# Performance work log

Hardware: AMD Instinct MI355X
Metric: run time of the kernel (lower is better)

Reference implementation:

```python
import jax, jax.numpy as jnp
import numpy as np

B, C, H, W = 4, 256, 64, 64


def setup_inputs() -> dict:
    key = jax.random.key(0)
    ks = jax.random.split(key, 7)
    s = 1.0 / np.sqrt(C)
    return {
        "x": jax.random.normal(ks[0], (B, C, H, W), jnp.float32),
        "context": jax.random.normal(ks[1], (B, C, H, W), jnp.float32),
        "wq": jax.random.normal(ks[2], (C, C), jnp.float32) * s,
        "bq": jnp.zeros((C,), jnp.float32),
        "wk": jax.random.normal(ks[3], (C, C), jnp.float32) * s,
        "bk": jnp.zeros((C,), jnp.float32),
        "wv": jax.random.normal(ks[4], (C, C), jnp.float32) * s,
        "bv": jnp.zeros((C,), jnp.float32),
        "wo": jax.random.normal(ks[5], (C, C), jnp.float32) * s,
        "bo": jnp.zeros((C,), jnp.float32),
    }


def _proj(w, b, feats):
    # 1x1 conv == channel-mixing linear: feats [B,C,N] -> [B,C,N]
    return jnp.einsum("oc,bcn->bon", w, feats) + b[None, :, None]


def reference(x, context, wq, bq, wk, bk, wv, bv, wo, bo):
    b, c, h, w = x.shape
    xf = x.reshape(b, c, h * w)              # [B,C,Nq]
    cf = context.reshape(b, c, -1)           # [B,C,Nk]
    q = _proj(wq, bq, xf)                    # [B,C,Nq]
    k = _proj(wk, bk, cf)                    # [B,C,Nk]
    v = _proj(wv, bv, cf)                    # [B,C,Nk]
    attn = jnp.einsum("bci,bcj->bij", q, k)  # [B,Nq,Nk] = q^T k
    attn = jax.nn.softmax(attn, axis=-1)
    out = jnp.einsum("bcj,bij->bci", v, attn)  # v @ attn^T, [B,C,Nq]
    out = _proj(wo, bo, out).reshape(b, c, h, w)
    return out + x
```

## Files before the change

### kernel.cpp

```cpp
#include <hip/hip_runtime.h>

typedef _Float16 f16;
typedef _Float16 f16x8 __attribute__((ext_vector_type(8)));
typedef _Float16 f16x4 __attribute__((ext_vector_type(4)));
typedef float f32x4 __attribute__((ext_vector_type(4)));

#define DEVI __device__ __forceinline__

constexpr int B_ = 4, C_ = 256, N_ = 4096;

#define MFMAH(a, b, c) __builtin_amdgcn_mfma_f32_16x16x32_f16((a), (b), (c), 0, 0, 0)

DEVI void gload16(const void* g, void* l) {
  __builtin_amdgcn_global_load_lds((const __attribute__((address_space(1))) void*)g,
                                   (__attribute__((address_space(3))) void*)l, 16, 0, 0);
}

DEVI float bcast_row(float v0, float v1, float v2, float v3, int l15) {
  int src = (l15 >> 2) << 4;
  float a0 = __shfl(v0, src, 64);
  float a1 = __shfl(v1, src, 64);
  float a2 = __shfl(v2, src, 64);
  float a3 = __shfl(v3, src, 64);
  float x0 = (l15 & 1) ? a1 : a0;
  float x1 = (l15 & 1) ? a3 : a2;
  return (l15 & 2) ? x1 : x0;
}

__global__ __launch_bounds__(256, 1) void prep_weights(
    const float* __restrict__ wq, const float* __restrict__ wk,
    const float* __restrict__ wv, const float* __restrict__ wo,
    f16* __restrict__ wqh, f16* __restrict__ wkh,
    f16* __restrict__ wvh, f16* __restrict__ woh) {
  int idx = blockIdx.x * 256 + threadIdx.x;
  wqh[idx] = (f16)wq[idx];
  wkh[idx] = (f16)wk[idx];
  wvh[idx] = (f16)wv[idx];
  woh[idx] = (f16)wo[idx];
}

__global__ __launch_bounds__(256, 2) void proj_kv(
    const float* __restrict__ ctx, const float* __restrict__ bk, const float* __restrict__ bv,
    const f16* __restrict__ wkh, const f16* __restrict__ wvh,
    f16* __restrict__ KTh, f16* __restrict__ Vg) {
  const int blk = blockIdx.x;
  const int b = blk & 3;
  const int j0 = (blk >> 2) << 6;
  const int tid = threadIdx.x;
  const int lane = tid & 63;
  const int w = tid >> 6;
  const int l15 = lane & 15;
  const int g = lane >> 4;

  __shared__ alignas(16) f16 ldsC[64 * 256];

  {
    const float* cb = ctx + (size_t)b * C_ * N_ + j0;
    #pragma unroll
    for (int it = 0; it < 16; ++it) {
      int idx = it * 256 + tid;
      int c = idx >> 4;
      int j4 = (idx & 15) << 2;
      float4 f = *(const float4*)(cb + (size_t)c * N_ + j4);
      float vv[4] = {f.x, f.y, f.z, f.w};
      #pragma unroll
      for (int e = 0; e < 4; ++e) {
        int j = j4 + e;
        int uidx = j * 256 + ((((c >> 3) ^ (j & 7))) << 3) + (c & 7);
        ldsC[uidx] = (f16)vv[e];
      }
    }
  }
  __syncthreads();

  const int jloc = 16 * w + l15;
  f16x8 ch[8];
  #pragma unroll
  for (int ks = 0; ks < 8; ++ks)
    ch[ks] = *(const f16x8*)&ldsC[jloc * 256 + (((g + 4 * ks) ^ (jloc & 7)) << 3)];

  #pragma unroll 4
  for (int mt = 0; mt < 16; ++mt) {
    f32x4 ka = {0, 0, 0, 0}, va = {0, 0, 0, 0};
    #pragma unroll
    for (int ks = 0; ks < 8; ++ks) {
      int aoff = (16 * mt + l15) * 256 + 8 * g + 32 * ks;
      f16x8 ah = *(const f16x8*)(wkh + aoff);
      f16x8 av = *(const f16x8*)(wvh + aoff);
      ka = MFMAH(ah, ch[ks], ka);
      va = MFMAH(av, ch[ks], va);
    }
    int c0 = 16 * mt + 4 * g;
    float4 bk4 = *(const float4*)(bk + c0);
    float4 bv4 = *(const float4*)(bv + c0);
    f16x4 h4;
    #pragma unroll
    for (int r = 0; r < 4; ++r) h4[r] = (f16)(ka[r] + ((const float*)&bk4)[r]);
    *(f16x4*)(KTh + ((size_t)b * N_ + j0 + jloc) * C_ + c0) = h4;
    #pragma unroll
    for (int r = 0; r < 4; ++r) {
      float vv = va[r] + ((const float*)&bv4)[r];
      Vg[((size_t)b * C_ + c0 + r) * N_ + j0 + jloc] = (f16)vv;
    }
  }
}

DEVI void stageK(const f16* khg, int kv0, f16* ldsK, int w, int lane) {
  #pragma unroll
  for (int t = 0; t < 8; ++t) {
    int L = t * 256 + w * 64 + lane;
    int j = L >> 5, s = L & 31;
    const f16* src = khg + (size_t)(kv0 + j) * C_ + ((s ^ (j & 7)) << 3);
    gload16(src, ldsK + (size_t)(t * 256 + w * 64) * 8);
  }
}
DEVI void stageV(const f16* vg, int kv0, f16* ldsV, int w, int lane) {
  #pragma unroll
  for (int t = 0; t < 8; ++t) {
    int L = t * 256 + w * 64 + lane;
    int c = L >> 3, sl = L & 7;
    const f16* src = vg + (size_t)c * N_ + kv0 + ((sl ^ (c & 7)) << 3);
    gload16(src, ldsV + (size_t)(t * 256 + w * 64) * 8);
  }
}

__global__ __launch_bounds__(256, 1) void attn_fused(
    const float* __restrict__ x, const float* __restrict__ bq, const float* __restrict__ bo,
    const f16* __restrict__ wqh, const f16* __restrict__ woh,
    const f16* __restrict__ KTh, const f16* __restrict__ Vg,
    float* __restrict__ out) {
  const int blk = blockIdx.x;
  const int b = (blk & 7) >> 1;
  const int i0 = (((blk >> 3) << 1) | (blk & 1)) << 6;
  const int tid = threadIdx.x;
  const int lane = tid & 63;
  const int w = tid >> 6;
  const int l15 = lane & 15;
  const int g = lane >> 4;

  __shared__ alignas(16) char smem[140288];
  f16* ldsK0 = (f16*)smem;
  f16* ldsK1 = (f16*)(smem + 32768);
  f16* ldsV0 = (f16*)(smem + 65536);
  f16* ldsV1 = (f16*)(smem + 98304);
  f16* ldsPT = (f16*)(smem + 131072);

  {
    const float* xb = x + (size_t)b * C_ * N_ + i0;
    #pragma unroll
    for (int it = 0; it < 16; ++it) {
      int idx = it * 256 + tid;
      int c = idx >> 4;
      int i4 = (idx & 15) << 2;
      float4 f = *(const float4*)(xb + (size_t)c * N_ + i4);
      float vv[4] = {f.x, f.y, f.z, f.w};
      #pragma unroll
      for (int e = 0; e < 4; ++e) {
        int i = i4 + e;
        int uidx = i * 256 + ((((c >> 3) ^ (i & 7))) << 3) + (c & 7);
        ldsK0[uidx] = (f16)vv[e];
      }
    }
  }
  __syncthreads();

  const int iloc = 16 * w + l15;

  f16x8 xh[8];
  #pragma unroll
  for (int ks = 0; ks < 8; ++ks)
    xh[ks] = *(const f16x8*)&ldsK0[iloc * 256 + (((g + 4 * ks) ^ (iloc & 7)) << 3)];

  f32x4 qd[16];
  #pragma unroll
  for (int mt = 0; mt < 16; ++mt) {
    f32x4 a1 = {0, 0, 0, 0};
    #pragma unroll
    for (int ks = 0; ks < 8; ++ks) {
      f16x8 ah = *(const f16x8*)(wqh + (16 * mt + l15) * 256 + 8 * g + 32 * ks);
      a1 = MFMAH(ah, xh[ks], a1);
    }
    int c0 = 16 * mt + 4 * g;
    float4 bq4 = *(const float4*)(bq + c0);
    #pragma unroll
    for (int r = 0; r < 4; ++r) qd[mt][r] = a1[r] + ((const float*)&bq4)[r];
  }
  __syncthreads();

  #pragma unroll
  for (int mt = 0; mt < 16; ++mt) {
    int c0 = 16 * mt + 4 * g;
    f16x4 h4;
    #pragma unroll
    for (int r = 0; r < 4; ++r) h4[r] = (f16)qd[mt][r];
    *(f16x4*)&ldsK0[iloc * 256 + ((((c0 >> 3) ^ (iloc & 7))) << 3) + (c0 & 7)] = h4;
  }
  __syncthreads();

  f16x8 qh[8];
  #pragma unroll
  for (int ks = 0; ks < 8; ++ks)
    qh[ks] = *(const f16x8*)&ldsK0[iloc * 256 + (((g + 4 * ks) ^ (iloc & 7)) << 3)];
  __syncthreads();

  const f16* khg = KTh + (size_t)b * N_ * C_;
  const f16* vg = Vg + (size_t)b * C_ * N_;

  float mrun[4] = {-1e30f, -1e30f, -1e30f, -1e30f};
  float lrun[4] = {0, 0, 0, 0};
  f32x4 oacc[16];
  #pragma unroll
  for (int mt = 0; mt < 16; ++mt) oacc[mt] = (f32x4){0, 0, 0, 0};

  stageK(khg, 0, ldsK0, w, lane);
  stageV(vg, 0, ldsV0, w, lane);
  __syncthreads();

  for (int t = 0; t < 64; ++t) {
    const int kv0 = t << 6;
    f16* Kc = (t & 1) ? ldsK1 : ldsK0;
    f16* Vc = (t & 1) ? ldsV1 : ldsV0;
    f16* Kn = (t & 1) ? ldsK0 : ldsK1;
    f16* Vn = (t & 1) ? ldsV0 : ldsV1;

    if (t < 63) {
      stageK(khg, kv0 + 64, Kn, w, lane);
      stageV(vg, kv0 + 64, Vn, w, lane);
    }

    f32x4 s1[4];
    #pragma unroll
    for (int nt = 0; nt < 4; ++nt) s1[nt] = (f32x4){0, 0, 0, 0};
    #pragma unroll
    for (int ks = 0; ks < 8; ++ks) {
      f16x8 bh[4];
      #pragma unroll
      for (int nt = 0; nt < 4; ++nt) {
        int j = 16 * nt + l15;
        bh[nt] = *(const f16x8*)&Kc[j * 256 + (((g + 4 * ks) ^ (j & 7)) << 3)];
      }
      #pragma unroll
      for (int nt = 0; nt < 4; ++nt) s1[nt] = MFMAH(qh[ks], bh[nt], s1[nt]);
    }

    float tm[4];
    #pragma unroll
    for (int r = 0; r < 4; ++r) {
      tm[r] = fmaxf(fmaxf(s1[0][r], s1[1][r]), fmaxf(s1[2][r], s1[3][r]));
      #pragma unroll
      for (int msk = 1; msk < 16; msk <<= 1) tm[r] = fmaxf(tm[r], __shfl_xor(tm[r], msk));
    }
    bool grow = (tm[0] > mrun[0] + 6.f) | (tm[1] > mrun[1] + 6.f) |
                (tm[2] > mrun[2] + 6.f) | (tm[3] > mrun[3] + 6.f);
    float sc[4] = {1.f, 1.f, 1.f, 1.f};
    int need = __any((int)grow);
    if (need) {
      #pragma unroll
      for (int r = 0; r < 4; ++r) {
        float mn = fmaxf(mrun[r], tm[r]);
        sc[r] = __expf(mrun[r] - mn);
        mrun[r] = mn;
      }
      float fsc = bcast_row(sc[0], sc[1], sc[2], sc[3], l15);
      #pragma unroll
      for (int mt = 0; mt < 16; ++mt) oacc[mt] *= fsc;
    }
    float rs[4] = {0, 0, 0, 0};
    #pragma unroll
    for (int nt = 0; nt < 4; ++nt) {
      #pragma unroll
      for (int r = 0; r < 4; ++r) {
        float p = __expf(s1[nt][r] - mrun[r]);
        s1[nt][r] = p;
        rs[r] += p;
      }
    }
    #pragma unroll
    for (int r = 0; r < 4; ++r) {
      #pragma unroll
      for (int msk = 1; msk < 16; msk <<= 1) rs[r] += __shfl_xor(rs[r], msk);
      lrun[r] = need ? lrun[r] * sc[r] + rs[r] : lrun[r] + rs[r];
    }

    #pragma unroll
    for (int nt = 0; nt < 4; ++nt) {
      int jcol = 16 * nt + l15;
      #pragma unroll
      for (int r = 0; r < 4; ++r) ldsPT[w * 1152 + (4 * g + r) * 72 + jcol] = (f16)s1[nt][r];
    }
    f16x8 pb[2];
    #pragma unroll
    for (int ks2 = 0; ks2 < 2; ++ks2)
      pb[ks2] = *(const f16x8*)&ldsPT[w * 1152 + l15 * 72 + 8 * (g + 4 * ks2)];

    #pragma unroll
    for (int ks2 = 0; ks2 < 2; ++ks2) {
      #pragma unroll
      for (int mt = 0; mt < 16; ++mt) {
        int c = 16 * mt + l15;
        f16x8 va = *(const f16x8*)&Vc[c * 64 + (((g + 4 * ks2) ^ (c & 7)) << 3)];
        oacc[mt] = MFMAH(va, pb[ks2], oacc[mt]);
      }
    }

    __syncthreads();
  }

  {
    float inv[4];
    #pragma unroll
    for (int r = 0; r < 4; ++r) inv[r] = 1.0f / lrun[r];
    float fi = bcast_row(inv[0], inv[1], inv[2], inv[3], l15);
    #pragma unroll
    for (int mt = 0; mt < 16; ++mt) oacc[mt] *= fi;
  }
  #pragma unroll
  for (int mt = 0; mt < 16; ++mt) {
    int c0 = 16 * mt + 4 * g;
    f16x4 h4;
    #pragma unroll
    for (int r = 0; r < 4; ++r) h4[r] = (f16)oacc[mt][r];
    *(f16x4*)&ldsK0[iloc * 256 + ((((c0 >> 3) ^ (iloc & 7))) << 3) + (c0 & 7)] = h4;
  }
  __syncthreads();
  f32x4 facc[16];
  #pragma unroll
  for (int mt = 0; mt < 16; ++mt) facc[mt] = (f32x4){0, 0, 0, 0};
  #pragma unroll
  for (int ks = 0; ks < 8; ++ks) {
    f16x8 ob = *(const f16x8*)&ldsK0[iloc * 256 + (((g + 4 * ks) ^ (iloc & 7)) << 3)];
    #pragma unroll
    for (int mt = 0; mt < 16; ++mt) {
      f16x8 ah = *(const f16x8*)(woh + (16 * mt + l15) * 256 + 8 * g + 32 * ks);
      facc[mt] = MFMAH(ah, ob, facc[mt]);
    }
  }
  const int ig = i0 + iloc;
  #pragma unroll
  for (int mt = 0; mt < 16; ++mt) {
    int c0 = 16 * mt + 4 * g;
    float4 bo4 = *(const float4*)(bo + c0);
    #pragma unroll
    for (int r = 0; r < 4; ++r) {
      size_t off = ((size_t)b * C_ + c0 + r) * N_ + ig;
      out[off] = facc[mt][r] + ((const float*)&bo4)[r] + x[off];
    }
  }
}

extern "C" void kernel_launch(void* const* d_in, const int* in_sizes, int n_in,
                              void* d_out, int out_size, void* d_ws, size_t ws_size,
                              hipStream_t stream) {
  const float* x = (const float*)d_in[0];
  const float* ctx = (const float*)d_in[1];
  const float* wq = (const float*)d_in[2];
  const float* bq = (const float*)d_in[3];
  const float* wk = (const float*)d_in[4];
  const float* bk = (const float*)d_in[5];
  const float* wv = (const float*)d_in[6];
  const float* bv = (const float*)d_in[7];
  const float* wo = (const float*)d_in[8];
  const float* bo = (const float*)d_in[9];
  float* out = (float*)d_out;

  f16* ws = (f16*)d_ws;
  f16* wqh = ws;
  f16* wkh = wqh + 65536;
  f16* wvh = wkh + 65536;
  f16* woh = wvh + 65536;
  f16* KTh = woh + 65536;
  f16* Vg = KTh + (size_t)B_ * N_ * C_;

  prep_weights<<<256, 256, 0, stream>>>(wq, wk, wv, wo, wqh, wkh, wvh, woh);
  proj_kv<<<256, 256, 0, stream>>>(ctx, bk, bv, wkh, wvh, KTh, Vg);
  attn_fused<<<256, 256, 0, stream>>>(x, bq, bo, wqh, woh, KTh, Vg, out);
}
```

Baseline: 354.6 us.

## Split attention output channels across wave pairs with 512-thread blocks

Doubles the attention block to 8 waves. Each pair of waves covers the same 16 query rows, and each wave in the pair owns half of the output channels for the Q projection, the PV accumulation and the output projection. The goal is better latency hiding, with two waves per SIMD instead of one, and fewer accumulator registers per wave. The cost is that both waves of a pair recompute the same QK^T scores and softmax, so score-side MFMA work is duplicated and the per-wave P scratch in LDS grows.

```diff
diff --git a/kernel.cpp b/kernel.cpp
--- a/kernel.cpp
+++ b/kernel.cpp
@@ -105,26 +105,26 @@
   }
 }
 
-DEVI void stageK(const f16* khg, int kv0, f16* ldsK, int w, int lane) {
-  #pragma unroll
-  for (int t = 0; t < 8; ++t) {
-    int L = t * 256 + w * 64 + lane;
+DEVI void stageK(const f16* khg, int kv0, f16* ldsK, int tid) {
+  #pragma unroll
+  for (int t = 0; t < 4; ++t) {
+    int L = t * 512 + tid;
     int j = L >> 5, s = L & 31;
     const f16* src = khg + (size_t)(kv0 + j) * C_ + ((s ^ (j & 7)) << 3);
-    gload16(src, ldsK + (size_t)(t * 256 + w * 64) * 8);
-  }
-}
-DEVI void stageV(const f16* vg, int kv0, f16* ldsV, int w, int lane) {
-  #pragma unroll
-  for (int t = 0; t < 8; ++t) {
-    int L = t * 256 + w * 64 + lane;
+    gload16(src, ldsK + (size_t)L * 8);
+  }
+}
+DEVI void stageV(const f16* vg, int kv0, f16* ldsV, int tid) {
+  #pragma unroll
+  for (int t = 0; t < 4; ++t) {
+    int L = t * 512 + tid;
     int c = L >> 3, sl = L & 7;
     const f16* src = vg + (size_t)c * N_ + kv0 + ((sl ^ (c & 7)) << 3);
-    gload16(src, ldsV + (size_t)(t * 256 + w * 64) * 8);
-  }
-}
-
-__global__ __launch_bounds__(256, 1) void attn_fused(
+    gload16(src, ldsV + (size_t)L * 8);
+  }
+}
+
+__global__ __launch_bounds__(512, 2) void attn_fused(
     const float* __restrict__ x, const float* __restrict__ bq, const float* __restrict__ bo,
     const f16* __restrict__ wqh, const f16* __restrict__ woh,
     const f16* __restrict__ KTh, const f16* __restrict__ Vg,
@@ -135,10 +135,12 @@
   const int tid = threadIdx.x;
   const int lane = tid & 63;
   const int w = tid >> 6;
+  const int h = w >> 2;
+  const int rg = w & 3;
   const int l15 = lane & 15;
   const int g = lane >> 4;
 
-  __shared__ alignas(16) char smem[140288];
+  __shared__ alignas(16) char smem[149504];
   f16* ldsK0 = (f16*)smem;
   f16* ldsK1 = (f16*)(smem + 32768);
   f16* ldsV0 = (f16*)(smem + 65536);
@@ -148,8 +150,8 @@
   {
     const float* xb = x + (size_t)b * C_ * N_ + i0;
     #pragma unroll
-    for (int it = 0; it < 16; ++it) {
-      int idx = it * 256 + tid;
+    for (int it = 0; it < 8; ++it) {
+      int idx = it * 512 + tid;
       int c = idx >> 4;
       int i4 = (idx & 15) << 2;
       float4 f = *(const float4*)(xb + (size_t)c * N_ + i4);
@@ -164,16 +166,17 @@
   }
   __syncthreads();
 
-  const int iloc = 16 * w + l15;
+  const int iloc = 16 * rg + l15;
 
   f16x8 xh[8];
   #pragma unroll
   for (int ks = 0; ks < 8; ++ks)
     xh[ks] = *(const f16x8*)&ldsK0[iloc * 256 + (((g + 4 * ks) ^ (iloc & 7)) << 3)];
 
-  f32x4 qd[16];
-  #pragma unroll
-  for (int mt = 0; mt < 16; ++mt) {
+  f32x4 qd[8];
+  #pragma unroll
+  for (int mtl = 0; mtl < 8; ++mtl) {
+    int mt = 8 * h + mtl;
     f32x4 a1 = {0, 0, 0, 0};
     #pragma unroll
     for (int ks = 0; ks < 8; ++ks) {
@@ -183,16 +186,16 @@
     int c0 = 16 * mt + 4 * g;
     float4 bq4 = *(const float4*)(bq + c0);
     #pragma unroll
-    for (int r = 0; r < 4; ++r) qd[mt][r] = a1[r] + ((const float*)&bq4)[r];
-  }
-  __syncthreads();
-
-  #pragma unroll
-  for (int mt = 0; mt < 16; ++mt) {
-    int c0 = 16 * mt + 4 * g;
+    for (int r = 0; r < 4; ++r) qd[mtl][r] = a1[r] + ((const float*)&bq4)[r];
+  }
+  __syncthreads();
+
+  #pragma unroll
+  for (int mtl = 0; mtl < 8; ++mtl) {
+    int c0 = 16 * (8 * h + mtl) + 4 * g;
     f16x4 h4;
     #pragma unroll
-    for (int r = 0; r < 4; ++r) h4[r] = (f16)qd[mt][r];
+    for (int r = 0; r < 4; ++r) h4[r] = (f16)qd[mtl][r];
     *(f16x4*)&ldsK0[iloc * 256 + ((((c0 >> 3) ^ (iloc & 7))) << 3) + (c0 & 7)] = h4;
   }
   __syncthreads();
@@ -208,12 +211,12 @@
 
   float mrun[4] = {-1e30f, -1e30f, -1e30f, -1e30f};
   float lrun[4] = {0, 0, 0, 0};
-  f32x4 oacc[16];
-  #pragma unroll
-  for (int mt = 0; mt < 16; ++mt) oacc[mt] = (f32x4){0, 0, 0, 0};
-
-  stageK(khg, 0, ldsK0, w, lane);
-  stageV(vg, 0, ldsV0, w, lane);
+  f32x4 oacc[8];
+  #pragma unroll
+  for (int mtl = 0; mtl < 8; ++mtl) oacc[mtl] = (f32x4){0, 0, 0, 0};
+
+  stageK(khg, 0, ldsK0, tid);
+  stageV(vg, 0, ldsV0, tid);
   __syncthreads();
 
   for (int t = 0; t < 64; ++t) {
@@ -224,8 +227,8 @@
     f16* Vn = (t & 1) ? ldsV0 : ldsV1;
 
     if (t < 63) {
-      stageK(khg, kv0 + 64, Kn, w, lane);
-      stageV(vg, kv0 + 64, Vn, w, lane);
+      stageK(khg, kv0 + 64, Kn, tid);
+      stageV(vg, kv0 + 64, Vn, tid);
     }
 
     f32x4 s1[4];
@@ -263,7 +266,7 @@
       }
       float fsc = bcast_row(sc[0], sc[1], sc[2], sc[3], l15);
       #pragma unroll
-      for (int mt = 0; mt < 16; ++mt) oacc[mt] *= fsc;
+      for (int mtl = 0; mtl < 8; ++mtl) oacc[mtl] *= fsc;
     }
     float rs[4] = {0, 0, 0, 0};
     #pragma unroll
@@ -296,10 +299,10 @@
     #pragma unroll
     for (int ks2 = 0; ks2 < 2; ++ks2) {
       #pragma unroll
-      for (int mt = 0; mt < 16; ++mt) {
-        int c = 16 * mt + l15;
+      for (int mtl = 0; mtl < 8; ++mtl) {
+        int c = 16 * (8 * h + mtl) + l15;
         f16x8 va = *(const f16x8*)&Vc[c * 64 + (((g + 4 * ks2) ^ (c & 7)) << 3)];
-        oacc[mt] = MFMAH(va, pb[ks2], oacc[mt]);
+        oacc[mtl] = MFMAH(va, pb[ks2], oacc[mtl]);
       }
     }
 
@@ -312,38 +315,38 @@
     for (int r = 0; r < 4; ++r) inv[r] = 1.0f / lrun[r];
     float fi = bcast_row(inv[0], inv[1], inv[2], inv[3], l15);
     #pragma unroll
-    for (int mt = 0; mt < 16; ++mt) oacc[mt] *= fi;
-  }
-  #pragma unroll
-  for (int mt = 0; mt < 16; ++mt) {
-    int c0 = 16 * mt + 4 * g;
+    for (int mtl = 0; mtl < 8; ++mtl) oacc[mtl] *= fi;
+  }
+  #pragma unroll
+  for (int mtl = 0; mtl < 8; ++mtl) {
+    int c0 = 16 * (8 * h + mtl) + 4 * g;
     f16x4 h4;
     #pragma unroll
-    for (int r = 0; r < 4; ++r) h4[r] = (f16)oacc[mt][r];
+    for (int r = 0; r < 4; ++r) h4[r] = (f16)oacc[mtl][r];
     *(f16x4*)&ldsK0[iloc * 256 + ((((c0 >> 3) ^ (iloc & 7))) << 3) + (c0 & 7)] = h4;
   }
   __syncthreads();
-  f32x4 facc[16];
-  #pragma unroll
-  for (int mt = 0; mt < 16; ++mt) facc[mt] = (f32x4){0, 0, 0, 0};
+  f32x4 facc[8];
+  #pragma unroll
+  for (int mtl = 0; mtl < 8; ++mtl) facc[mtl] = (f32x4){0, 0, 0, 0};
   #pragma unroll
   for (int ks = 0; ks < 8; ++ks) {
     f16x8 ob = *(const f16x8*)&ldsK0[iloc * 256 + (((g + 4 * ks) ^ (iloc & 7)) << 3)];
     #pragma unroll
-    for (int mt = 0; mt < 16; ++mt) {
-      f16x8 ah = *(const f16x8*)(woh + (16 * mt + l15) * 256 + 8 * g + 32 * ks);
-      facc[mt] = MFMAH(ah, ob, facc[mt]);
+    for (int mtl = 0; mtl < 8; ++mtl) {
+      f16x8 ah = *(const f16x8*)(woh + (16 * (8 * h + mtl) + l15) * 256 + 8 * g + 32 * ks);
+      facc[mtl] = MFMAH(ah, ob, facc[mtl]);
     }
   }
   const int ig = i0 + iloc;
   #pragma unroll
-  for (int mt = 0; mt < 16; ++mt) {
-    int c0 = 16 * mt + 4 * g;
+  for (int mtl = 0; mtl < 8; ++mtl) {
+    int c0 = 16 * (8 * h + mtl) + 4 * g;
     float4 bo4 = *(const float4*)(bo + c0);
     #pragma unroll
     for (int r = 0; r < 4; ++r) {
       size_t off = ((size_t)b * C_ + c0 + r) * N_ + ig;
-      out[off] = facc[mt][r] + ((const float*)&bo4)[r] + x[off];
+      out[off] = facc[mtl][r] + ((const float*)&bo4)[r] + x[off];
     }
   }
 }
@@ -373,5 +376,5 @@
 
   prep_weights<<<256, 256, 0, stream>>>(wq, wk, wv, wo, wqh, wkh, wvh, woh);
   proj_kv<<<256, 256, 0, stream>>>(ctx, bk, bv, wkh, wvh, KTh, Vg);
-  attn_fused<<<256, 256, 0, stream>>>(x, bq, bo, wqh, woh, KTh, Vg, out);
-}
+  attn_fused<<<256, 512, 0, stream>>>(x, bq, bo, wqh, woh, KTh, Vg, out);
+}
```

Result: no change. 361.3 us (+1.9%).
